# Performance work log

Measured on AMD Instinct MI355X. Metric: run time of the kernel, lower is better.

The kernel has to match this reference:

```python
import jax, jax.numpy as jnp
import numpy as np

EPS = 1e-5


def _mamba(x, in_w, conv_w, conv_b, x_w, dt_w, dt_b, A_log, D, out_w):
    # x: [B, L, d_model] -> [B, L, d_model]; mamba_ssm defaults (bias-free in/out proj)
    Bsz, L, _ = x.shape
    d_inner, d_conv = conv_w.shape
    dt_rank = dt_w.shape[1]
    N = A_log.shape[1]

    xz = x @ in_w.T                              # [B, L, 2*d_inner]
    u, z = jnp.split(xz, 2, axis=-1)

    # causal depthwise conv (torch pads both sides by d_conv-1 then slices [:L])
    uc = jnp.pad(u.transpose(0, 2, 1), ((0, 0), (0, 0), (d_conv - 1, 0)))  # [B, d, L+pad]
    uc = jax.lax.conv_general_dilated(
        uc, conv_w[:, None, :], window_strides=(1,), padding='VALID',
        feature_group_count=d_inner, dimension_numbers=('NCH', 'OIH', 'NCH'))
    u = jax.nn.silu(uc + conv_b[None, :, None]).transpose(0, 2, 1)          # [B, L, d]

    xdbc = u @ x_w.T                              # [B, L, dt_rank + 2N]
    dt, Bm, Cm = jnp.split(xdbc, [dt_rank, dt_rank + N], axis=-1)
    delta = jax.nn.softplus(dt @ dt_w.T + dt_b)   # [B, L, d]

    A = -jnp.exp(A_log)                           # [d, N]
    dA = jnp.exp(delta[..., None] * A)            # [B, L, d, N]
    dBu = delta[..., None] * Bm[:, :, None, :] * u[..., None]  # [B, L, d, N]

    def step(h, inp):
        dA_t, dBu_t, C_t = inp
        h = dA_t * h + dBu_t                      # [B, d, N]
        y = jnp.einsum('bdn,bn->bd', h, C_t)
        return h, y

    h0 = jnp.zeros((Bsz, d_inner, N), dA.dtype)
    _, ys = jax.lax.scan(step, h0,
                         (dA.transpose(1, 0, 2, 3), dBu.transpose(1, 0, 2, 3), Cm.transpose(1, 0, 2)))
    y = ys.transpose(1, 0, 2)                     # [B, L, d]
    y = (y + u * D) * jax.nn.silu(z)
    return y @ out_w.T


def reference(x, input_lengths, m, emb, conv_w, conv_b, ln_g, ln_b,
              f_in_w, f_conv_w, f_conv_b, f_x_w, f_dt_w, f_dt_b, f_A_log, f_D, f_out_w,
              b_in_w, b_conv_w, b_conv_b, b_x_w, b_dt_w, b_dt_b, b_A_log, b_D, b_out_w,
              proj_w, proj_b):
    K = conv_w.shape[-1]
    pad = (K - 1) // 2
    h = emb[x].transpose(0, 2, 1)                 # [B, C, L]
    for i in range(conv_w.shape[0]):
        h = jax.lax.conv_general_dilated(h, conv_w[i], (1,), [(pad, pad)],
                                         dimension_numbers=('NCH', 'OIH', 'NCH'))
        h = h + conv_b[i][None, :, None]
        mu = h.mean(axis=1, keepdims=True)
        var = ((h - mu) ** 2).mean(axis=1, keepdims=True)
        h = (h - mu) * jax.lax.rsqrt(var + EPS)
        h = h * ln_g[i][None, :, None] + ln_b[i][None, :, None]
        h = jnp.where(h > 0, h, 0.2 * h)          # LeakyReLU(0.2); dropout is eval no-op
        h = jnp.where(m[:, None, :], 0.0, h)
    h = h.transpose(0, 2, 1)                      # [B, L, C]
    fo = _mamba(h, f_in_w, f_conv_w, f_conv_b, f_x_w, f_dt_w, f_dt_b, f_A_log, f_D, f_out_w)
    bo = _mamba(h[:, ::-1], b_in_w, b_conv_w, b_conv_b, b_x_w, b_dt_w, b_dt_b, b_A_log, b_D, b_out_w)
    comb = jnp.concatenate([fo, bo], axis=-1) @ proj_w.T + proj_b
    return jnp.where(m[:, :, None], 0.0, comb)


def setup_inputs() -> dict:
    key = jax.random.key(0)
    ks = iter(jax.random.split(key, 40))
    B, L, C, K, depth, V = 4, 1024, 512, 5, 3, 178
    d_inner, d_state, d_conv, dt_rank = 2 * C, 16, 4, 32
    inp = {
        'x': jax.random.randint(next(ks), (B, L), 0, V),
        'input_lengths': jax.random.randint(next(ks), (B,), 1, L + 1),
        'm': jnp.zeros((B, L), dtype=bool),
        'emb': jax.random.normal(next(ks), (V, C)),
        'conv_w': jax.random.normal(next(ks), (depth, C, C, K)) * 0.05,
        'conv_b': jax.random.normal(next(ks), (depth, C)) * 0.05,
        'ln_g': jnp.ones((depth, C)),
        'ln_b': jnp.zeros((depth, C)),
        'proj_w': jax.random.normal(next(ks), (C, 2 * C)) * 0.02,
        'proj_b': jax.random.normal(next(ks), (C,)) * 0.02,
    }
    for p in ('f', 'b'):
        inp[p + '_in_w'] = jax.random.normal(next(ks), (2 * d_inner, C)) * 0.02
        inp[p + '_conv_w'] = jax.random.normal(next(ks), (d_inner, d_conv)) * 0.1
        inp[p + '_conv_b'] = jax.random.normal(next(ks), (d_inner,)) * 0.1
        inp[p + '_x_w'] = jax.random.normal(next(ks), (dt_rank + 2 * d_state, d_inner)) * 0.02
        inp[p + '_dt_w'] = jax.random.normal(next(ks), (d_inner, dt_rank)) * 0.02
        inp[p + '_dt_b'] = jax.random.normal(next(ks), (d_inner,)) * 0.1
        inp[p + '_A_log'] = jax.random.uniform(next(ks), (d_inner, d_state))
        inp[p + '_D'] = jax.random.normal(next(ks), (d_inner,)) * 0.1
        inp[p + '_out_w'] = jax.random.normal(next(ks), (C, d_inner)) * 0.02
    return inp
```

## Files before the change

kernel.cpp:

```cpp
#include <hip/hip_runtime.h>
#include <hip/hip_bf16.h>

typedef __attribute__((ext_vector_type(8))) short short8;
typedef __attribute__((ext_vector_type(4))) float f32x4;
typedef __attribute__((ext_vector_type(4))) unsigned short ushort4_t;

#define BSZ 4
#define LSEQ 1024
#define CCH 512
#define BL (BSZ*LSEQ)
#define BL2 (2*BL)
#define DI 1024
#define NST 16
#define DTR 32
#define NCH 32
#define CLEN 32

__device__ __forceinline__ float sigmoidf_(float x){ return 1.f/(1.f+__expf(-x)); }
__device__ __forceinline__ float softplus_(float x){ return x > 20.f ? x : __logf(1.f + __expf(x)); }
__device__ __forceinline__ float fexp2_(float x){ return __builtin_amdgcn_exp2f(x); }
__device__ __forceinline__ unsigned short f2bf_(float f){
  __hip_bfloat16 h = __float2bfloat16(f); return *(unsigned short*)&h;
}
__device__ __forceinline__ float b2f_(unsigned short s){
  unsigned u = ((unsigned)s) << 16; float f; __builtin_memcpy(&f, &u, 4); return f;
}

typedef const __attribute__((address_space(1))) unsigned int* gas_t;
typedef __attribute__((address_space(3))) unsigned int* las_t;
__device__ __forceinline__ void gload16(const void* g, void* l){
  __builtin_amdgcn_global_load_lds((gas_t)g, (las_t)l, 16, 0, 0);
}


struct CastEnt { const float* s; unsigned short* d; unsigned n4, acc; };
struct CastArgs { CastEnt e[9]; unsigned total4; };
__global__ void k_cast_all(CastArgs a){
  unsigned i = blockIdx.x*256 + threadIdx.x;
  if (i >= a.total4) return;
  #pragma unroll
  for (int k=0;k<9;k++){
    if (i < a.e[k].acc + a.e[k].n4){
      unsigned j = i - a.e[k].acc;
      float4 v = ((const float4*)a.e[k].s)[j];
      ushort4_t o = { f2bf_(v.x), f2bf_(v.y), f2bf_(v.z), f2bf_(v.w) };
      *(ushort4_t*)(a.e[k].d + (size_t)j*4) = o;
      return;
    }
  }
}

__global__ void k_prep_convw(const float* __restrict__ cw, __hip_bfloat16* __restrict__ wt){
  int i = blockIdx.x*256 + threadIdx.x;
  const int total = 3*CCH*CCH*5;
  if (i >= total) return;
  int j = i % (CCH*5);
  int co = (i/(CCH*5)) % CCH;
  int layer = i/(CCH*5*CCH);
  int k = j >> 9, ci = j & 511;
  wt[i] = __float2bfloat16(cw[(((size_t)layer*CCH + co)*CCH + ci)*5 + k]);
}

__global__ void k_embed(const int* __restrict__ x, const float* __restrict__ emb,
                        __hip_bfloat16* __restrict__ xpad0, __hip_bfloat16* __restrict__ xpad1){
  int i = blockIdx.x*256 + threadIdx.x;
  const int total = BSZ*(LSEQ+4)*CCH;
  const int total2 = total + BSZ*4*CCH;
  if (i >= total2) return;
  if (i >= total){
    int j = i - total;
    int c = j & (CCH-1);
    int pr = (j >> 9) & 3;
    int b = j >> 11;
    int rr = (pr < 2) ? pr : (LSEQ+2) + (pr-2);
    xpad1[((size_t)b*(LSEQ+4) + rr)*CCH + c] = __float2bfloat16(0.f);
    return;
  }
  int c = i & (CCH-1);
  int r = (i >> 9) % (LSEQ+4);
  int b = i / ((LSEQ+4)*CCH);
  float v = 0.f;
  if (r >= 2 && r < LSEQ+2){
    int tok = x[b*LSEQ + (r-2)];
    v = emb[(size_t)tok*CCH + c];
  }
  xpad0[i] = __float2bfloat16(v);
}

__global__ __launch_bounds__(256) void k_ln(
    const float* __restrict__ in, const float* __restrict__ in2,
    const float* __restrict__ g, const float* __restrict__ bb,
    const unsigned char* __restrict__ mask,
    __hip_bfloat16* __restrict__ xpad_next,
    __hip_bfloat16* __restrict__ h_enc, __hip_bfloat16* __restrict__ h_rev){
  int row = blockIdx.x;
  int b = row >> 10, l = row & 1023;
  const float* xr = in + (size_t)row*CCH;
  const float* xr2 = in2 + (size_t)row*CCH;
  int t = threadIdx.x;
  float v0 = xr[t] + xr2[t], v1 = xr[t+256] + xr2[t+256];
  float s = v0+v1, s2 = v0*v0 + v1*v1;
  #pragma unroll
  for (int off=32; off>0; off>>=1){ s += __shfl_down(s,off); s2 += __shfl_down(s2,off); }
  __shared__ float ls[8];
  if ((t&63)==0){ ls[t>>6] = s; ls[(t>>6)+4] = s2; }
  __syncthreads();
  float S  = ls[0]+ls[1]+ls[2]+ls[3];
  float S2 = ls[4]+ls[5]+ls[6]+ls[7];
  float mu = S*(1.f/CCH);
  float var = S2*(1.f/CCH) - mu*mu;
  float rs = rsqrtf(var + 1e-5f);
  bool mk = mask[row] != 0;
  #pragma unroll
  for (int e=0; e<2; e++){
    int c = t + e*256;
    float v = e ? v1 : v0;
    float h = (v-mu)*rs*g[c] + bb[c];
    h = h > 0.f ? h : 0.2f*h;
    if (mk) h = 0.f;
    __hip_bfloat16 hb = __float2bfloat16(h);
    if (xpad_next) xpad_next[((size_t)b*(LSEQ+4) + (l+2))*CCH + c] = hb;
    if (h_enc) h_enc[(size_t)row*CCH + c] = hb;
    if (h_rev) h_rev[((size_t)(b<<10) + (1023-l))*CCH + c] = hb;
  }
}

__global__ __launch_bounds__(256) void k_gemm_ksplit(
    const __hip_bfloat16* __restrict__ A, int lda,
    const __hip_bfloat16* __restrict__ W, size_t wStride,
    float* __restrict__ Cout, int ldc, int K, unsigned short* __restrict__ dtb){
  __shared__ float red[4*1024];
  int m0 = blockIdx.x << 4;
  const __hip_bfloat16* Wd = W + (size_t)(m0 >> 12)*wStride;
  int tid = threadIdx.x;
  int w = tid >> 6, lane = tid & 63;
  int r = lane & 15, kg = lane >> 4;
  int Kw = K >> 2;
  int kbase = w*Kw;

  const short* Ap = (const short*)A + (size_t)(m0 + r)*lda + kbase + kg*8;
  const short* Wp[4];
  #pragma unroll
  for (int nj=0; nj<4; nj++)
    Wp[nj] = (const short*)Wd + (size_t)(nj*16 + r)*K + kbase + kg*8;

  f32x4 acc[4];
  #pragma unroll
  for (int nj=0;nj<4;nj++) acc[nj] = (f32x4){0.f,0.f,0.f,0.f};

  for (int kk=0; kk<Kw; kk+=32){
    short8 a = *(const short8*)(Ap + kk);
    #pragma unroll
    for (int nj=0;nj<4;nj++){
      short8 wv = *(const short8*)(Wp[nj] + kk);
      acc[nj] = __builtin_amdgcn_mfma_f32_16x16x32_bf16(a, wv, acc[nj], 0,0,0);
    }
  }
  #pragma unroll
  for (int nj=0;nj<4;nj++)
    #pragma unroll
    for (int reg=0; reg<4; reg++){
      int rowt = kg*4 + reg;
      int col  = nj*16 + r;
      red[w*1024 + rowt*64 + col] = acc[nj][reg];
    }
  __syncthreads();
  int e0 = tid*4;
  f32x4 s = *(const f32x4*)&red[e0];
  #pragma unroll
  for (int ww=1; ww<4; ww++){
    f32x4 p = *(const f32x4*)&red[ww*1024 + e0];
    s.x += p.x; s.y += p.y; s.z += p.z; s.w += p.w;
  }
  int rowt = e0 >> 6, col = e0 & 63;
  *(f32x4*)&Cout[(size_t)(m0+rowt)*ldc + col] = s;
  if (col < 32){
    ushort4_t o = { f2bf_(s.x), f2bf_(s.y), f2bf_(s.z), f2bf_(s.w) };
    *(ushort4_t*)&dtb[(size_t)(m0+rowt)*32 + col] = o;
  }
}

template<bool OUTBF>
__global__ __launch_bounds__(256) void k_gemm_big(
    const __hip_bfloat16* __restrict__ A, int lda, int padExtra,
    const __hip_bfloat16* __restrict__ W, size_t wStride,
    void* __restrict__ C0, void* __restrict__ C1, size_t segBytes, int ldc, int coloff,
    int tiles_n, int baseBlocks, int totalBlocks, int Kc, int Kb,
    const float* __restrict__ bias, int biasStride, int act,
    const unsigned char* __restrict__ mask, int outRowSub, int dirColOff, int uzMode){
  __shared__ alignas(16) __hip_bfloat16 smem[3][6144];
  int b = blockIdx.x;
  int wg = (b & 7)*(totalBlocks >> 3) + (b >> 3);
  int seg = wg / baseBlocks;
  int bid = wg - seg*baseBlocks;
  int tn = bid % tiles_n;
  int tm = bid / tiles_n;
  int m0 = tm*128, n0 = tn*64;
  int dir = m0 >> 12;
  int kOff = seg*Kc;
  const __hip_bfloat16* Wd = W + (size_t)dir*wStride;
  void* Cout = (void*)((char*)C0 + (size_t)seg*segBytes);
  const float* biasp = (bias && seg==0) ? bias + dir*biasStride : nullptr;

  int tid = threadIdx.x;
  int wid = tid >> 6, lane = tid & 63;
  int r = lane & 15, kg = lane >> 4;

  int sr = lane >> 2;
  int gs = (lane & 3) ^ ((sr >> 1) & 3);
  int arow0 = m0 + wid*16 + sr;
  int arow1 = arow0 + 64;
  int pa0 = arow0 + padExtra*(arow0 >> 10);
  int pa1 = arow1 + padExtra*(arow1 >> 10);
  size_t aoff0 = (size_t)pa0*lda + kOff + gs*8;
  size_t aoff1 = (size_t)pa1*lda + kOff + gs*8;
  int bcol = n0 + wid*16 + sr;
  size_t boff = (size_t)bcol*Kb + kOff + gs*8;

  int wr = wid >> 1, wc = wid & 1;
  int xs = (kg ^ ((r >> 1) & 3))*8;
  int afrag[4], bfrag[2];
  #pragma unroll
  for (int mi=0; mi<4; mi++) afrag[mi] = (wr*64 + mi*16 + r)*32 + xs;
  #pragma unroll
  for (int nj=0; nj<2; nj++) bfrag[nj] = 4096 + (wc*32 + nj*16 + r)*32 + xs;

  f32x4 acc[4][2];
  #pragma unroll
  for (int mi=0;mi<4;mi++)
    #pragma unroll
    for (int nj=0;nj<2;nj++) acc[mi][nj] = (f32x4){0.f,0.f,0.f,0.f};

  const int nt = Kc >> 5;
  auto stage = [&](int kt, int bufi){
    __hip_bfloat16* sb = &smem[bufi][0];
    int k0 = kt*32;
    gload16((const short*)A + aoff0 + k0, sb + wid*512);
    gload16((const short*)A + aoff1 + k0, sb + (wid+4)*512);
    gload16((const short*)W + (size_t)(Wd - W) + boff + k0, sb + 4096 + wid*512);
  };
  auto compute = [&](int bufi){
    const __hip_bfloat16* sb = &smem[bufi][0];
    short8 a[4], bb2[2];
    #pragma unroll
    for (int mi=0;mi<4;mi++) a[mi] = *(const short8*)&sb[afrag[mi]];
    #pragma unroll
    for (int nj=0;nj<2;nj++) bb2[nj] = *(const short8*)&sb[bfrag[nj]];
    #pragma unroll
    for (int mi=0;mi<4;mi++)
      #pragma unroll
      for (int nj=0;nj<2;nj++)
        acc[mi][nj] = __builtin_amdgcn_mfma_f32_16x16x32_bf16(a[mi], bb2[nj], acc[mi][nj], 0,0,0);
  };

  if (nt >= 3){
    stage(0, 0);
    stage(1, 1);
    int bi = 0;
    #pragma unroll 1
    for (int t=0; t<nt; t++){
      if (t+1 < nt) asm volatile("s_waitcnt vmcnt(3)" ::: "memory");
      else          asm volatile("s_waitcnt vmcnt(0)" ::: "memory");
      __builtin_amdgcn_s_barrier();
      __builtin_amdgcn_sched_barrier(0);
      if (t+2 < nt){
        int nb2 = bi + 2; if (nb2 >= 3) nb2 -= 3;
        stage(t+2, nb2);
      }
      compute(bi);
      bi = (bi+1 == 3) ? 0 : bi+1;
    }
  } else {
    for (int s=0; s<nt; s++) stage(s, s);
    asm volatile("s_waitcnt vmcnt(0)" ::: "memory");
    __builtin_amdgcn_s_barrier();
    __builtin_amdgcn_sched_barrier(0);
    for (int t=0; t<nt; t++) compute(t);
  }

  #pragma unroll
  for (int mi=0;mi<4;mi++){
    #pragma unroll
    for (int nj=0;nj<2;nj++){
      #pragma unroll
      for (int reg=0; reg<4; reg++){
        int row = m0 + wr*64 + mi*16 + kg*4 + reg;
        int col = n0 + wc*32 + nj*16 + r;
        float v = acc[mi][nj][reg];
        if (uzMode){
          if (col < 1024) ((__hip_bfloat16*)C0)[(size_t)row*1024 + col] = __float2bfloat16(v);
          else            ((float*)C1)[(size_t)row*1024 + (col-1024)] = v;
          continue;
        }
        if (biasp) v += biasp[col];
        if (act == 1) v = softplus_(v);
        int row_out = row - dir*outRowSub;
        if (mask && mask[row_out]) v = 0.f;
        size_t o = (size_t)row_out*ldc + coloff + dir*dirColOff + col;
        if (OUTBF) ((__hip_bfloat16*)Cout)[o] = __float2bfloat16(v);
        else       ((float*)Cout)[o] = v;
      }
    }
  }
}


__global__ void k_dwconv(const unsigned short* __restrict__ upre,
                         const float* __restrict__ cw0, const float* __restrict__ cw1,
                         const float* __restrict__ cb0, const float* __restrict__ cb1,
                         float* __restrict__ u, __hip_bfloat16* __restrict__ ub){
  int i = blockIdx.x*256 + threadIdx.x;
  if (i >= BL2*DI/4) return;
  int d4 = i & (DI/4 - 1);
  int d = d4 << 2;
  int row = i >> 8;
  int dir = row >> 12;
  const float* cw = (dir ? cw1 : cw0) + d*4;
  const float* cb = (dir ? cb1 : cb0) + d;
  int l = row & 1023;
  int rb = row & ~1023;
  f32x4 cwv[4];
  #pragma unroll
  for (int j=0;j<4;j++) cwv[j] = *(const f32x4*)&cw[j*4];
  f32x4 acc = *(const f32x4*)cb;
  #pragma unroll
  for (int k=0;k<4;k++){
    int ll = l - 3 + k;
    if (ll >= 0){
      ushort4_t xv = *(const ushort4_t*)&upre[(size_t)(rb + ll)*DI + d];
      acc.x = __fmaf_rn(cwv[0][k], b2f_(xv.x), acc.x);
      acc.y = __fmaf_rn(cwv[1][k], b2f_(xv.y), acc.y);
      acc.z = __fmaf_rn(cwv[2][k], b2f_(xv.z), acc.z);
      acc.w = __fmaf_rn(cwv[3][k], b2f_(xv.w), acc.w);
    }
  }
  f32x4 s;
  s.x = acc.x * sigmoidf_(acc.x);
  s.y = acc.y * sigmoidf_(acc.y);
  s.z = acc.z * sigmoidf_(acc.z);
  s.w = acc.w * sigmoidf_(acc.w);
  *(f32x4*)&u[(size_t)i*4] = s;
  ushort4_t o = { f2bf_(s.x), f2bf_(s.y), f2bf_(s.z), f2bf_(s.w) };
  *(ushort4_t*)((unsigned short*)ub + (size_t)i*4) = o;
}


__global__ __launch_bounds__(256) void k_scan_part(
    const float* __restrict__ Alog0, const float* __restrict__ Alog1,
    const float* __restrict__ dy, const float* __restrict__ u,
    const float* __restrict__ xdbc,
    float* __restrict__ Hp, float* __restrict__ Pp){
  __shared__ alignas(16) float Bsh[CLEN*16];
  int t = threadIdx.x;
  int dblk = blockIdx.x & 3;
  int c = (blockIdx.x >> 2) & (NCH-1);
  int b8 = blockIdx.x >> 7;
  const float* A_log = (b8 >> 2) ? Alog1 : Alog0;
  int d = dblk*256 + t;
  size_t blbase = (size_t)b8*LSEQ + (size_t)c*CLEN;
  if (t < CLEN*4){
    int l = t >> 2, q = t & 3;
    *(f32x4*)&Bsh[l*16 + q*4] = *(const f32x4*)&xdbc[(blbase+l)*64 + 32 + q*4];
  }
  float Af[16];
  #pragma unroll
  for (int n=0; n<16; n+=4){
    f32x4 a = *(const f32x4*)&A_log[(size_t)d*16 + n];
    Af[n]   = -__expf(a.x)*1.442695041f; Af[n+1] = -__expf(a.y)*1.442695041f;
    Af[n+2] = -__expf(a.z)*1.442695041f; Af[n+3] = -__expf(a.w)*1.442695041f;
  }
  float h[16];
  #pragma unroll
  for (int n=0;n<16;n++) h[n]=0.f;
  float Sdv = 0.f;
  const float* dyp = dy + blbase*DI + d;
  const float* up  = u  + blbase*DI + d;
  float dvb[2][8], uvb[2][8];
  #pragma unroll
  for (int j=0;j<8;j++){ dvb[0][j] = dyp[(size_t)j*DI]; uvb[0][j] = up[(size_t)j*DI]; }
  __syncthreads();
  #pragma unroll
  for (int g=0; g<4; g++){
    int cur = g & 1;
    if (g+1 < 4){
      int nxt = cur ^ 1;
      #pragma unroll
      for (int j=0;j<8;j++){
        size_t l = (size_t)(g+1)*8 + j;
        dvb[nxt][j] = dyp[l*DI]; uvb[nxt][j] = up[l*DI];
      }
    }
    #pragma unroll
    for (int j=0;j<8;j++){
      int l = g*8 + j;
      float dv = dvb[cur][j], uv = uvb[cur][j];
      float duv = dv*uv;
      Sdv += dv;
      #pragma unroll
      for (int n=0;n<16;n++){
        float dA = fexp2_(dv*Af[n]);
        h[n] = __fmaf_rn(dA, h[n], duv*Bsh[l*16+n]);
      }
    }
  }
  size_t pb = (((size_t)(b8*NCH + c))*DI + d)*16;
  #pragma unroll
  for (int n=0;n<16;n+=4){
    *(f32x4*)&Hp[pb+n] = (f32x4){h[n],h[n+1],h[n+2],h[n+3]};
    *(f32x4*)&Pp[pb+n] = (f32x4){fexp2_(Af[n]*Sdv), fexp2_(Af[n+1]*Sdv),
                                 fexp2_(Af[n+2]*Sdv), fexp2_(Af[n+3]*Sdv)};
  }
}

__global__ void k_scan_comb(float* __restrict__ Hp, float* __restrict__ Pp){
  int i = blockIdx.x*256 + threadIdx.x;
  if (i >= BL2*NST) return;
  int n = i & 15, row = i >> 4;
  int b8 = row >> 10, d = row & 1023;
  float hin = 0.f;
  #pragma unroll
  for (int c=0;c<NCH;c++){
    size_t idx = (((size_t)(b8*NCH + c))*DI + d)*16 + n;
    float P = Pp[idx], H = Hp[idx];
    Pp[idx] = hin;
    hin = __fmaf_rn(P, hin, H);
  }
}

__global__ __launch_bounds__(256) void k_scan_fin(
    const float* __restrict__ Alog0, const float* __restrict__ Alog1,
    const float* __restrict__ dy, const float* __restrict__ u,
    const float* __restrict__ xdbc,
    const float* __restrict__ Hin, const float* __restrict__ zf,
    const float* __restrict__ Dp0, const float* __restrict__ Dp1,
    __hip_bfloat16* __restrict__ yb){
  __shared__ alignas(16) float BCsh[CLEN*32];
  int t = threadIdx.x;
  int dblk = blockIdx.x & 3;
  int c = (blockIdx.x >> 2) & (NCH-1);
  int b8 = blockIdx.x >> 7;
  int dirb = b8 >> 2;
  const float* A_log = dirb ? Alog1 : Alog0;
  const float* Dp = dirb ? Dp1 : Dp0;
  int d = dblk*256 + t;
  size_t blbase = (size_t)b8*LSEQ + (size_t)c*CLEN;
  {
    int l = t >> 3, q = t & 7;
    *(f32x4*)&BCsh[l*32 + q*4] = *(const f32x4*)&xdbc[(blbase+l)*64 + 32 + q*4];
  }
  float Af[16];
  #pragma unroll
  for (int n=0; n<16; n+=4){
    f32x4 a = *(const f32x4*)&A_log[(size_t)d*16 + n];
    Af[n]   = -__expf(a.x)*1.442695041f; Af[n+1] = -__expf(a.y)*1.442695041f;
    Af[n+2] = -__expf(a.z)*1.442695041f; Af[n+3] = -__expf(a.w)*1.442695041f;
  }
  size_t pb = (((size_t)(b8*NCH + c))*DI + d)*16;
  float h[16];
  #pragma unroll
  for (int n=0;n<16;n+=4){
    f32x4 hv = *(const f32x4*)&Hin[pb+n];
    h[n]=hv.x; h[n+1]=hv.y; h[n+2]=hv.z; h[n+3]=hv.w;
  }
  float Dd = Dp[d];
  const float* dyp = dy + blbase*DI + d;
  const float* up  = u  + blbase*DI + d;
  const float* zp  = zf + blbase*DI + d;
  float dvb[2][8], uvb[2][8], zvb[2][8];
  #pragma unroll
  for (int j=0;j<8;j++){
    dvb[0][j] = dyp[(size_t)j*DI];
    uvb[0][j] = up[(size_t)j*DI];
    zvb[0][j] = zp[(size_t)j*DI];
  }
  __syncthreads();
  #pragma unroll
  for (int g=0; g<4; g++){
    int cur = g & 1;
    if (g+1 < 4){
      int nxt = cur ^ 1;
      #pragma unroll
      for (int j=0;j<8;j++){
        size_t l = (size_t)(g+1)*8 + j;
        dvb[nxt][j] = dyp[l*DI];
        uvb[nxt][j] = up[l*DI];
        zvb[nxt][j] = zp[l*DI];
      }
    }
    #pragma unroll
    for (int j=0;j<8;j++){
      int l = g*8 + j;
      float dv = dvb[cur][j], uv = uvb[cur][j], zv = zvb[cur][j];
      float duv = dv*uv;
      float y = 0.f;
      #pragma unroll
      for (int n=0;n<16;n++){
        float dA = fexp2_(dv*Af[n]);
        h[n] = __fmaf_rn(dA, h[n], duv*BCsh[l*32+n]);
        y = __fmaf_rn(h[n], BCsh[l*32+16+n], y);
      }
      float gg = zv * sigmoidf_(zv);
      float out = __fmaf_rn(uv, Dd, y) * gg;
      yb[(blbase+l)*DI + d] = __float2bfloat16(out);
    }
  }
}


extern "C" void kernel_launch(void* const* d_in, const int* in_sizes, int n_in,
                              void* d_out, int out_size, void* d_ws, size_t ws_size,
                              hipStream_t stream){
  (void)in_sizes; (void)n_in; (void)out_size; (void)ws_size;
  const int*   x     = (const int*)d_in[0];
  const unsigned char* m = (const unsigned char*)d_in[2];
  const float* emb   = (const float*)d_in[3];
  const float* convw = (const float*)d_in[4];
  const float* convb = (const float*)d_in[5];
  const float* lng   = (const float*)d_in[6];
  const float* lnb   = (const float*)d_in[7];
  const float* projw = (const float*)d_in[8];
  const float* projb = (const float*)d_in[9];

  char* ws = (char*)d_ws;
  size_t off = 0;
  auto alloc = [&](size_t bytes)->char*{
    char* p = ws + off; off += (bytes + 255) & ~((size_t)255); return p;
  };
  auto wt_conv = (__hip_bfloat16*)alloc((size_t)3*CCH*CCH*5*2);
  auto w_in2  = (__hip_bfloat16*)alloc((size_t)2*2*DI*CCH*2);
  auto w_x2   = (__hip_bfloat16*)alloc((size_t)2*64*DI*2);
  auto w_dt2  = (__hip_bfloat16*)alloc((size_t)2*DI*DTR*2);
  auto w_out2 = (__hip_bfloat16*)alloc((size_t)2*CCH*DI*2);
  auto w_proj = (__hip_bfloat16*)alloc((size_t)CCH*1024*2);
  auto dtbias2= (float*)alloc((size_t)2*DI*4);
  auto xpad0  = (__hip_bfloat16*)alloc((size_t)BSZ*(LSEQ+4)*CCH*2);
  auto xpad1  = (__hip_bfloat16*)alloc((size_t)BSZ*(LSEQ+4)*CCH*2);
  auto scr    = (float*)alloc((size_t)8*NCH*DI*NST*4);
  auto h_cat  = (__hip_bfloat16*)alloc((size_t)BL2*CCH*2);
  auto upre   = (unsigned short*)alloc((size_t)BL2*DI*2);
  auto zf     = (float*)alloc((size_t)BL2*DI*4);
  auto u2     = (float*)alloc((size_t)BL2*DI*4);
  auto ub2    = (__hip_bfloat16*)alloc((size_t)BL2*DI*2);
  auto xdbc2  = (float*)alloc((size_t)BL2*64*4);
  auto dtb2   = (unsigned short*)alloc((size_t)BL2*DTR*2);
  auto dy2    = (float*)alloc((size_t)BL2*DI*4);
  auto yb2    = (__hip_bfloat16*)alloc((size_t)BL2*DI*2);
  auto fob    = (__hip_bfloat16*)alloc((size_t)BL*DI*2);
  auto Pp     = (float*)alloc((size_t)8*NCH*DI*NST*4);

  float* Hp = scr;

  auto nb = [](size_t n){ return (unsigned)((n + 255)/256); };

  k_prep_convw<<<dim3(nb((size_t)3*CCH*CCH*5)), dim3(256), 0, stream>>>(convw, wt_conv);
  {
    CastArgs ca;
    unsigned acc = 0;
    auto put = [&](int k, const void* s, void* d, unsigned n4){
      ca.e[k].s = (const float*)s; ca.e[k].d = (unsigned short*)d;
      ca.e[k].n4 = n4; ca.e[k].acc = acc; acc += n4;
    };
    for (int dir=0; dir<2; dir++){
      int base = 10 + 9*dir;
      put(dir*4+0, d_in[base+0], (unsigned short*)w_in2  + (size_t)dir*2*DI*CCH, (2*DI*CCH)/4);
      put(dir*4+1, d_in[base+3], (unsigned short*)w_x2   + (size_t)dir*64*DI,    (64*DI)/4);
      put(dir*4+2, d_in[base+4], (unsigned short*)w_dt2  + (size_t)dir*DI*DTR,   (DI*DTR)/4);
      put(dir*4+3, d_in[base+8], (unsigned short*)w_out2 + (size_t)dir*CCH*DI,   (CCH*DI)/4);
    }
    put(8, projw, w_proj, (CCH*1024)/4);
    ca.total4 = acc;
    k_cast_all<<<dim3(nb(acc)), dim3(256), 0, stream>>>(ca);
  }
  hipMemcpyAsync(dtbias2,      d_in[15], DI*sizeof(float), hipMemcpyDeviceToDevice, stream);
  hipMemcpyAsync(dtbias2 + DI, d_in[24], DI*sizeof(float), hipMemcpyDeviceToDevice, stream);

  auto gemm_big = [&](const void* A, int lda, int padE, const void* W, size_t wStride,
                  void* C0, void* C1, size_t segBytes, int ldc, int coloff,
                  int M, int N, int Kc, int Kb, int nSeg,
                  const float* bias, int biasStride, int act,
                  const unsigned char* msk, int outRowSub, int dirColOff, bool outbf, int uzMode){
    int tiles_n = N/64;
    int baseBlocks = (M/128)*tiles_n;
    int blocks = baseBlocks * nSeg;
    if (outbf)
      k_gemm_big<true><<<dim3(blocks), dim3(256), 0, stream>>>((const __hip_bfloat16*)A, lda, padE,
          (const __hip_bfloat16*)W, wStride, C0, C1, segBytes, ldc, coloff, tiles_n, baseBlocks, blocks,
          Kc, Kb, bias, biasStride, act, msk, outRowSub, dirColOff, uzMode);
    else
      k_gemm_big<false><<<dim3(blocks), dim3(256), 0, stream>>>((const __hip_bfloat16*)A, lda, padE,
          (const __hip_bfloat16*)W, wStride, C0, C1, segBytes, ldc, coloff, tiles_n, baseBlocks, blocks,
          Kc, Kb, bias, biasStride, act, msk, outRowSub, dirColOff, uzMode);
  };

  k_embed<<<dim3(nb((size_t)BSZ*(LSEQ+4)*CCH + BSZ*4*CCH)), dim3(256), 0, stream>>>(x, emb, xpad0, xpad1);

  __hip_bfloat16* xp_in = xpad0;
  __hip_bfloat16* xp_out = xpad1;
  __hip_bfloat16* h_rev = h_cat + (size_t)BL*CCH;
  const size_t segB_conv = (size_t)((char*)dy2 - (char*)scr);
  for (int layer=0; layer<3; layer++){
    const __hip_bfloat16* wt = wt_conv + (size_t)layer*CCH*CCH*5;
    gemm_big(xp_in, CCH, 4, wt, 0, scr, nullptr, segB_conv, CCH, 0, BL, CCH, 1280, 2560, 2,
             convb + layer*CCH, 0, 0, nullptr, 0, 0, false, 0);
    bool last = (layer==2);
    k_ln<<<dim3(BL), dim3(256), 0, stream>>>(scr, dy2, lng + layer*CCH, lnb + layer*CCH, m,
        last ? nullptr : xp_out, last ? h_cat : nullptr, last ? h_rev : nullptr);
    __hip_bfloat16* t2 = xp_in; xp_in = xp_out; xp_out = t2;
  }

  const float* Alog0 = (const float*)d_in[16];
  const float* Alog1 = (const float*)d_in[25];
  const float* Dp0   = (const float*)d_in[17];
  const float* Dp1   = (const float*)d_in[26];

  gemm_big(h_cat, CCH, 0, w_in2, (size_t)2*DI*CCH, upre, zf, 0, 2*DI, 0,
           BL2, 2*DI, CCH, CCH, 1, nullptr, 0, 0, nullptr, 0, 0, false, 1);
  k_dwconv<<<dim3(nb((size_t)BL2*DI/4)), dim3(256), 0, stream>>>(upre,
      (const float*)d_in[11], (const float*)d_in[20],
      (const float*)d_in[12], (const float*)d_in[21], u2, ub2);
  k_gemm_ksplit<<<dim3(BL2/16), dim3(256), 0, stream>>>(ub2, DI, w_x2, (size_t)64*DI, xdbc2, 64, DI, dtb2);
  gemm_big(dtb2, DTR, 0, w_dt2, (size_t)DI*DTR, dy2, nullptr, 0, DI, 0,
           BL2, DI, DTR, DTR, 1, dtbias2, DI, 1, nullptr, 0, 0, false, 0);
  k_scan_part<<<dim3(1024), dim3(256), 0, stream>>>(Alog0, Alog1, dy2, u2, xdbc2, Hp, Pp);
  k_scan_comb<<<dim3(nb((size_t)BL2*NST)), dim3(256), 0, stream>>>(Hp, Pp);
  k_scan_fin<<<dim3(1024), dim3(256), 0, stream>>>(Alog0, Alog1, dy2, u2, xdbc2, Pp, zf, Dp0, Dp1, yb2);
  gemm_big(yb2, DI, 0, w_out2, (size_t)CCH*DI, fob, nullptr, 0, DI, 0,
           BL2, CCH, DI, DI, 1, nullptr, 0, 0, nullptr, BL, 512, true, 0);

  gemm_big(fob, DI, 0, w_proj, 0, d_out, nullptr, 0, CCH, 0,
           BL, CCH, DI, DI, 1, projb, 0, 0, m, 0, 0, false, 0);
}
```

Before: 324.4 us.

## Drop fp32 u buffer, read reversed rows in GEMM, pass dt bias pointers directly

The scan kernels now read the bf16 copy of the conv output instead of a separate fp32 buffer, so the fp32 u write and its two reads go away. The backward-direction input is no longer materialised by the LayerNorm kernel. The in-projection GEMM instead maps its A rows in reverse for the second direction. The dt bias is passed as two pointers, which removes two device-to-device memcpys. The trade-off is that u in the scan is rounded to bf16, a small precision loss.

```diff
diff --git a/kernel.cpp b/kernel.cpp
--- a/kernel.cpp
+++ b/kernel.cpp
@@ -92,7 +92,7 @@
     const float* __restrict__ g, const float* __restrict__ bb,
     const unsigned char* __restrict__ mask,
     __hip_bfloat16* __restrict__ xpad_next,
-    __hip_bfloat16* __restrict__ h_enc, __hip_bfloat16* __restrict__ h_rev){
+    __hip_bfloat16* __restrict__ h_enc){
   int row = blockIdx.x;
   int b = row >> 10, l = row & 1023;
   const float* xr = in + (size_t)row*CCH;
@@ -121,7 +121,6 @@
     __hip_bfloat16 hb = __float2bfloat16(h);
     if (xpad_next) xpad_next[((size_t)b*(LSEQ+4) + (l+2))*CCH + c] = hb;
     if (h_enc) h_enc[(size_t)row*CCH + c] = hb;
-    if (h_rev) h_rev[((size_t)(b<<10) + (1023-l))*CCH + c] = hb;
   }
 }
 
@@ -182,11 +181,11 @@
 
 template<bool OUTBF>
 __global__ __launch_bounds__(256) void k_gemm_big(
-    const __hip_bfloat16* __restrict__ A, int lda, int padExtra,
+    const __hip_bfloat16* __restrict__ A, int lda, int padExtra, int revA,
     const __hip_bfloat16* __restrict__ W, size_t wStride,
     void* __restrict__ C0, void* __restrict__ C1, size_t segBytes, int ldc, int coloff,
     int tiles_n, int baseBlocks, int totalBlocks, int Kc, int Kb,
-    const float* __restrict__ bias, int biasStride, int act,
+    const float* __restrict__ bias0, const float* __restrict__ bias1, int act,
     const unsigned char* __restrict__ mask, int outRowSub, int dirColOff, int uzMode){
   __shared__ alignas(16) __hip_bfloat16 smem[3][6144];
   int b = blockIdx.x;
@@ -200,7 +199,8 @@
   int kOff = seg*Kc;
   const __hip_bfloat16* Wd = W + (size_t)dir*wStride;
   void* Cout = (void*)((char*)C0 + (size_t)seg*segBytes);
-  const float* biasp = (bias && seg==0) ? bias + dir*biasStride : nullptr;
+  const float* bsel = dir ? bias1 : bias0;
+  const float* biasp = (bsel && seg==0) ? bsel : nullptr;
 
   int tid = threadIdx.x;
   int wid = tid >> 6, lane = tid & 63;
@@ -208,12 +208,17 @@
 
   int sr = lane >> 2;
   int gs = (lane & 3) ^ ((sr >> 1) & 3);
+  auto physrow = [&](int ar)->int{
+    if (revA && ar >= 4096){
+      int r2 = ar - 4096;
+      return (r2 & ~1023) | (1023 - (r2 & 1023));
+    }
+    return ar + padExtra*(ar >> 10);
+  };
   int arow0 = m0 + wid*16 + sr;
   int arow1 = arow0 + 64;
-  int pa0 = arow0 + padExtra*(arow0 >> 10);
-  int pa1 = arow1 + padExtra*(arow1 >> 10);
-  size_t aoff0 = (size_t)pa0*lda + kOff + gs*8;
-  size_t aoff1 = (size_t)pa1*lda + kOff + gs*8;
+  size_t aoff0 = (size_t)physrow(arow0)*lda + kOff + gs*8;
+  size_t aoff1 = (size_t)physrow(arow1)*lda + kOff + gs*8;
   int bcol = n0 + wid*16 + sr;
   size_t boff = (size_t)bcol*Kb + kOff + gs*8;
 
@@ -308,7 +313,7 @@
 __global__ void k_dwconv(const unsigned short* __restrict__ upre,
                          const float* __restrict__ cw0, const float* __restrict__ cw1,
                          const float* __restrict__ cb0, const float* __restrict__ cb1,
-                         float* __restrict__ u, __hip_bfloat16* __restrict__ ub){
+                         __hip_bfloat16* __restrict__ ub){
   int i = blockIdx.x*256 + threadIdx.x;
   if (i >= BL2*DI/4) return;
   int d4 = i & (DI/4 - 1);
@@ -339,7 +344,6 @@
   s.y = acc.y * sigmoidf_(acc.y);
   s.z = acc.z * sigmoidf_(acc.z);
   s.w = acc.w * sigmoidf_(acc.w);
-  *(f32x4*)&u[(size_t)i*4] = s;
   ushort4_t o = { f2bf_(s.x), f2bf_(s.y), f2bf_(s.z), f2bf_(s.w) };
   *(ushort4_t*)((unsigned short*)ub + (size_t)i*4) = o;
 }
@@ -347,7 +351,7 @@
 
 __global__ __launch_bounds__(256) void k_scan_part(
     const float* __restrict__ Alog0, const float* __restrict__ Alog1,
-    const float* __restrict__ dy, const float* __restrict__ u,
+    const float* __restrict__ dy, const unsigned short* __restrict__ ub,
     const float* __restrict__ xdbc,
     float* __restrict__ Hp, float* __restrict__ Pp){
   __shared__ alignas(16) float Bsh[CLEN*16];
@@ -374,10 +378,10 @@
   for (int n=0;n<16;n++) h[n]=0.f;
   float Sdv = 0.f;
   const float* dyp = dy + blbase*DI + d;
-  const float* up  = u  + blbase*DI + d;
+  const unsigned short* ubp = ub + blbase*DI + d;
   float dvb[2][8], uvb[2][8];
   #pragma unroll
-  for (int j=0;j<8;j++){ dvb[0][j] = dyp[(size_t)j*DI]; uvb[0][j] = up[(size_t)j*DI]; }
+  for (int j=0;j<8;j++){ dvb[0][j] = dyp[(size_t)j*DI]; uvb[0][j] = b2f_(ubp[(size_t)j*DI]); }
   __syncthreads();
   #pragma unroll
   for (int g=0; g<4; g++){
@@ -387,7 +391,7 @@
       #pragma unroll
       for (int j=0;j<8;j++){
         size_t l = (size_t)(g+1)*8 + j;
-        dvb[nxt][j] = dyp[l*DI]; uvb[nxt][j] = up[l*DI];
+        dvb[nxt][j] = dyp[l*DI]; uvb[nxt][j] = b2f_(ubp[l*DI]);
       }
     }
     #pragma unroll
@@ -429,7 +433,7 @@
 
 __global__ __launch_bounds__(256) void k_scan_fin(
     const float* __restrict__ Alog0, const float* __restrict__ Alog1,
-    const float* __restrict__ dy, const float* __restrict__ u,
+    const float* __restrict__ dy, const unsigned short* __restrict__ ub,
     const float* __restrict__ xdbc,
     const float* __restrict__ Hin, const float* __restrict__ zf,
     const float* __restrict__ Dp0, const float* __restrict__ Dp1,
@@ -464,13 +468,13 @@
   }
   float Dd = Dp[d];
   const float* dyp = dy + blbase*DI + d;
-  const float* up  = u  + blbase*DI + d;
+  const unsigned short* ubp = ub + blbase*DI + d;
   const float* zp  = zf + blbase*DI + d;
   float dvb[2][8], uvb[2][8], zvb[2][8];
   #pragma unroll
   for (int j=0;j<8;j++){
     dvb[0][j] = dyp[(size_t)j*DI];
-    uvb[0][j] = up[(size_t)j*DI];
+    uvb[0][j] = b2f_(ubp[(size_t)j*DI]);
     zvb[0][j] = zp[(size_t)j*DI];
   }
   __syncthreads();
@@ -483,7 +487,7 @@
       for (int j=0;j<8;j++){
         size_t l = (size_t)(g+1)*8 + j;
         dvb[nxt][j] = dyp[l*DI];
-        uvb[nxt][j] = up[l*DI];
+        uvb[nxt][j] = b2f_(ubp[l*DI]);
         zvb[nxt][j] = zp[l*DI];
       }
     }
@@ -532,14 +536,12 @@
   auto w_dt2  = (__hip_bfloat16*)alloc((size_t)2*DI*DTR*2);
   auto w_out2 = (__hip_bfloat16*)alloc((size_t)2*CCH*DI*2);
   auto w_proj = (__hip_bfloat16*)alloc((size_t)CCH*1024*2);
-  auto dtbias2= (float*)alloc((size_t)2*DI*4);
   auto xpad0  = (__hip_bfloat16*)alloc((size_t)BSZ*(LSEQ+4)*CCH*2);
   auto xpad1  = (__hip_bfloat16*)alloc((size_t)BSZ*(LSEQ+4)*CCH*2);
   auto scr    = (float*)alloc((size_t)8*NCH*DI*NST*4);
-  auto h_cat  = (__hip_bfloat16*)alloc((size_t)BL2*CCH*2);
+  auto h_enc  = (__hip_bfloat16*)alloc((size_t)BL*CCH*2);
   auto upre   = (unsigned short*)alloc((size_t)BL2*DI*2);
   auto zf     = (float*)alloc((size_t)BL2*DI*4);
-  auto u2     = (float*)alloc((size_t)BL2*DI*4);
   auto ub2    = (__hip_bfloat16*)alloc((size_t)BL2*DI*2);
   auto xdbc2  = (float*)alloc((size_t)BL2*64*4);
   auto dtb2   = (unsigned short*)alloc((size_t)BL2*DTR*2);
@@ -571,40 +573,37 @@
     ca.total4 = acc;
     k_cast_all<<<dim3(nb(acc)), dim3(256), 0, stream>>>(ca);
   }
-  hipMemcpyAsync(dtbias2,      d_in[15], DI*sizeof(float), hipMemcpyDeviceToDevice, stream);
-  hipMemcpyAsync(dtbias2 + DI, d_in[24], DI*sizeof(float), hipMemcpyDeviceToDevice, stream);
-
-  auto gemm_big = [&](const void* A, int lda, int padE, const void* W, size_t wStride,
+
+  auto gemm_big = [&](const void* A, int lda, int padE, int revA, const void* W, size_t wStride,
                   void* C0, void* C1, size_t segBytes, int ldc, int coloff,
                   int M, int N, int Kc, int Kb, int nSeg,
-                  const float* bias, int biasStride, int act,
+                  const float* bias0, const float* bias1, int act,
                   const unsigned char* msk, int outRowSub, int dirColOff, bool outbf, int uzMode){
     int tiles_n = N/64;
     int baseBlocks = (M/128)*tiles_n;
     int blocks = baseBlocks * nSeg;
     if (outbf)
-      k_gemm_big<true><<<dim3(blocks), dim3(256), 0, stream>>>((const __hip_bfloat16*)A, lda, padE,
+      k_gemm_big<true><<<dim3(blocks), dim3(256), 0, stream>>>((const __hip_bfloat16*)A, lda, padE, revA,
           (const __hip_bfloat16*)W, wStride, C0, C1, segBytes, ldc, coloff, tiles_n, baseBlocks, blocks,
-          Kc, Kb, bias, biasStride, act, msk, outRowSub, dirColOff, uzMode);
+          Kc, Kb, bias0, bias1, act, msk, outRowSub, dirColOff, uzMode);
     else
-      k_gemm_big<false><<<dim3(blocks), dim3(256), 0, stream>>>((const __hip_bfloat16*)A, lda, padE,
+      k_gemm_big<false><<<dim3(blocks), dim3(256), 0, stream>>>((const __hip_bfloat16*)A, lda, padE, revA,
           (const __hip_bfloat16*)W, wStride, C0, C1, segBytes, ldc, coloff, tiles_n, baseBlocks, blocks,
-          Kc, Kb, bias, biasStride, act, msk, outRowSub, dirColOff, uzMode);
+          Kc, Kb, bias0, bias1, act, msk, outRowSub, dirColOff, uzMode);
   };
 
   k_embed<<<dim3(nb((size_t)BSZ*(LSEQ+4)*CCH + BSZ*4*CCH)), dim3(256), 0, stream>>>(x, emb, xpad0, xpad1);
 
   __hip_bfloat16* xp_in = xpad0;
   __hip_bfloat16* xp_out = xpad1;
-  __hip_bfloat16* h_rev = h_cat + (size_t)BL*CCH;
   const size_t segB_conv = (size_t)((char*)dy2 - (char*)scr);
   for (int layer=0; layer<3; layer++){
     const __hip_bfloat16* wt = wt_conv + (size_t)layer*CCH*CCH*5;
-    gemm_big(xp_in, CCH, 4, wt, 0, scr, nullptr, segB_conv, CCH, 0, BL, CCH, 1280, 2560, 2,
-             convb + layer*CCH, 0, 0, nullptr, 0, 0, false, 0);
+    gemm_big(xp_in, CCH, 4, 0, wt, 0, scr, nullptr, segB_conv, CCH, 0, BL, CCH, 1280, 2560, 2,
+             convb + layer*CCH, convb + layer*CCH, 0, nullptr, 0, 0, false, 0);
     bool last = (layer==2);
     k_ln<<<dim3(BL), dim3(256), 0, stream>>>(scr, dy2, lng + layer*CCH, lnb + layer*CCH, m,
-        last ? nullptr : xp_out, last ? h_cat : nullptr, last ? h_rev : nullptr);
+        last ? nullptr : xp_out, last ? h_enc : nullptr);
     __hip_bfloat16* t2 = xp_in; xp_in = xp_out; xp_out = t2;
   }
 
@@ -613,20 +612,21 @@
   const float* Dp0   = (const float*)d_in[17];
   const float* Dp1   = (const float*)d_in[26];
 
-  gemm_big(h_cat, CCH, 0, w_in2, (size_t)2*DI*CCH, upre, zf, 0, 2*DI, 0,
-           BL2, 2*DI, CCH, CCH, 1, nullptr, 0, 0, nullptr, 0, 0, false, 1);
+  gemm_big(h_enc, CCH, 0, 1, w_in2, (size_t)2*DI*CCH, upre, zf, 0, 2*DI, 0,
+           BL2, 2*DI, CCH, CCH, 1, nullptr, nullptr, 0, nullptr, 0, 0, false, 1);
   k_dwconv<<<dim3(nb((size_t)BL2*DI/4)), dim3(256), 0, stream>>>(upre,
       (const float*)d_in[11], (const float*)d_in[20],
-      (const float*)d_in[12], (const float*)d_in[21], u2, ub2);
+      (const float*)d_in[12], (const float*)d_in[21], ub2);
   k_gemm_ksplit<<<dim3(BL2/16), dim3(256), 0, stream>>>(ub2, DI, w_x2, (size_t)64*DI, xdbc2, 64, DI, dtb2);
-  gemm_big(dtb2, DTR, 0, w_dt2, (size_t)DI*DTR, dy2, nullptr, 0, DI, 0,
-           BL2, DI, DTR, DTR, 1, dtbias2, DI, 1, nullptr, 0, 0, false, 0);
-  k_scan_part<<<dim3(1024), dim3(256), 0, stream>>>(Alog0, Alog1, dy2, u2, xdbc2, Hp, Pp);
+  gemm_big(dtb2, DTR, 0, 0, w_dt2, (size_t)DI*DTR, dy2, nullptr, 0, DI, 0,
+           BL2, DI, DTR, DTR, 1, (const float*)d_in[15], (const float*)d_in[24], 1,
+           nullptr, 0, 0, false, 0);
+  k_scan_part<<<dim3(1024), dim3(256), 0, stream>>>(Alog0, Alog1, dy2, (const unsigned short*)ub2, xdbc2, Hp, Pp);
   k_scan_comb<<<dim3(nb((size_t)BL2*NST)), dim3(256), 0, stream>>>(Hp, Pp);
-  k_scan_fin<<<dim3(1024), dim3(256), 0, stream>>>(Alog0, Alog1, dy2, u2, xdbc2, Pp, zf, Dp0, Dp1, yb2);
-  gemm_big(yb2, DI, 0, w_out2, (size_t)CCH*DI, fob, nullptr, 0, DI, 0,
-           BL2, CCH, DI, DI, 1, nullptr, 0, 0, nullptr, BL, 512, true, 0);
-
-  gemm_big(fob, DI, 0, w_proj, 0, d_out, nullptr, 0, CCH, 0,
-           BL, CCH, DI, DI, 1, projb, 0, 0, m, 0, 0, false, 0);
-}
+  k_scan_fin<<<dim3(1024), dim3(256), 0, stream>>>(Alog0, Alog1, dy2, (const unsigned short*)ub2, xdbc2, Pp, zf, Dp0, Dp1, yb2);
+  gemm_big(yb2, DI, 0, 0, w_out2, (size_t)CCH*DI, fob, nullptr, 0, DI, 0,
+           BL2, CCH, DI, DI, 1, nullptr, nullptr, 0, nullptr, BL, 512, true, 0);
+
+  gemm_big(fob, DI, 0, 0, w_proj, 0, d_out, nullptr, 0, CCH, 0,
+           BL, CCH, DI, DI, 1, projb, projb, 0, m, 0, 0, false, 0);
+}
```

After: 311.6 us. -4.0%, faster.
